# Performance work log

Measured on AMD Instinct MI355X. Metric: run time of the kernel, lower is better.

The kernel has to match this reference:

```python
import jax, jax.numpy as jnp
import numpy as np

B, S, D = 2, 2048, 2048
H, HD = 16, 128
WINDOW = 512
ROPE_BASE = 10000.0


def setup_inputs() -> dict:
    key = jax.random.key(0)
    k1, k2, k3 = jax.random.split(key, 3)
    x = jax.random.normal(k1, (B, S, D), dtype=jnp.float32)
    w_qkv = jax.random.normal(k2, (3 * D, D), dtype=jnp.float32) * (D ** -0.5)
    w_out = jax.random.normal(k3, (D, D), dtype=jnp.float32) * (D ** -0.5)
    return {"x": x, "w_qkv": w_qkv, "w_out": w_out}


def _rope_cos_sin(seq_len, head_dim, base, dtype):
    inv_freq = 1.0 / (base ** (jnp.arange(0, head_dim, 2, dtype=jnp.float32) / head_dim))
    pos = jnp.arange(seq_len, dtype=jnp.float32)
    freqs = pos[:, None] * inv_freq[None, :]            # (S, HD/2)
    emb = jnp.concatenate([freqs, freqs], axis=-1)       # (S, HD)
    return jnp.cos(emb).astype(dtype), jnp.sin(emb).astype(dtype)


def _rotate_half(x):
    x1, x2 = jnp.split(x, 2, axis=-1)
    return jnp.concatenate([-x2, x1], axis=-1)


def reference(x, w_qkv, w_out):
    Bx, Sx, Dx = x.shape
    # fused QKV projection (torch Linear: x @ W^T)
    qkv = jnp.einsum('bsd,ed->bse', x, w_qkv)
    q, k, v = jnp.split(qkv, 3, axis=-1)
    q = q.reshape(Bx, Sx, H, HD).transpose(0, 2, 1, 3)   # (B,H,S,HD)
    k = k.reshape(Bx, Sx, H, HD).transpose(0, 2, 1, 3)
    v = v.reshape(Bx, Sx, H, HD).transpose(0, 2, 1, 3)
    # RoPE with implicit position_ids = arange(S)
    cos, sin = _rope_cos_sin(Sx, HD, ROPE_BASE, x.dtype)  # (S, HD)
    q = q * cos[None, None] + _rotate_half(q) * sin[None, None]
    k = k * cos[None, None] + _rotate_half(k) * sin[None, None]
    # sliding-window attention: attend iff 0 <= i - j < WINDOW
    scale = 1.0 / jnp.sqrt(jnp.array(HD, dtype=x.dtype))
    scores = jnp.einsum('bhqd,bhkd->bhqk', q, k) * scale
    i = jnp.arange(Sx)[:, None]
    j = jnp.arange(Sx)[None, :]
    diff = i - j
    valid = (diff >= 0) & (diff < WINDOW)                # (S, S)
    scores = jnp.where(valid[None, None], scores, jnp.finfo(scores.dtype).min)
    attn = jax.nn.softmax(scores, axis=-1)
    out = jnp.einsum('bhqk,bhkd->bhqd', attn, v)
    out = out.transpose(0, 2, 1, 3).reshape(Bx, Sx, Dx)
    return jnp.einsum('bsd,ed->bse', out, w_out)
```

## Files before the change

### kernel.cpp

```cpp
#include <hip/hip_runtime.h>

#define S_LEN 2048
#define DIM 2048
#define NH 16
#define HD 128
#define WIN 512
#define QKVD (3 * DIM)

typedef unsigned short u16;
typedef unsigned int u32;
typedef __bf16 bf16x8 __attribute__((ext_vector_type(8)));
typedef float f32x4 __attribute__((ext_vector_type(4)));

__device__ __forceinline__ u16 f2bf(float f) {
  unsigned u = __builtin_bit_cast(unsigned, f);
  u += 0x7FFFu + ((u >> 16) & 1u);
  return (u16)(u >> 16);
}
__device__ __forceinline__ float bf2f(u16 b) {
  return __builtin_bit_cast(float, (unsigned)b << 16);
}
__device__ __forceinline__ void async16(const void* g, void* l) {
  __builtin_amdgcn_global_load_lds((__attribute__((address_space(1))) void*)g,
                                   (__attribute__((address_space(3))) void*)l,
                                   16, 0, 0);
}
#define WAITV(N) asm volatile("s_waitcnt vmcnt(" #N ")" ::: "memory")

__global__ __launch_bounds__(256) void cvt3_kernel(
    const float* __restrict__ a, u16* __restrict__ oa, int na,
    const float* __restrict__ b, u16* __restrict__ ob, int nb,
    const float* __restrict__ c, u16* __restrict__ oc, int nc) {
  int i = (blockIdx.x * 256 + threadIdx.x) * 4;
  const float* src;
  u16* dst;
  if (i < na) { src = a + i; dst = oa + i; }
  else if (i < na + nb) { src = b + (i - na); dst = ob + (i - na); }
  else if (i < na + nb + nc) { src = c + (i - na - nb); dst = oc + (i - na - nb); }
  else return;
  float4 v = *(const float4*)src;
  ushort4 o;
  o.x = f2bf(v.x); o.y = f2bf(v.y); o.z = f2bf(v.z); o.w = f2bf(v.w);
  *(ushort4*)dst = o;
}

__global__ __launch_bounds__(256) void rope_tab_kernel(float* __restrict__ cosT,
                                                       float* __restrict__ sinT) {
  int idx = blockIdx.x * 256 + threadIdx.x;
  int s = idx >> 6, j = idx & 63;
  double freq = exp((double)j * -0.14391156831212787);
  double a = (double)s * freq;
  cosT[idx] = (float)cos(a);
  sinT[idx] = (float)sin(a);
}

template <int BN, typename TO>
__global__ __launch_bounds__(512, 2) void gemm8(const u16* __restrict__ A,
                                                const u16* __restrict__ B,
                                                TO* __restrict__ C,
                                                int M, int N, int K) {
  constexpr int ABY = 128 * 128;
  constexpr int BBY = BN * 128;
  constexpr int BLO = BN / 128;
  __shared__ __align__(16) char Al[2 * ABY];
  __shared__ __align__(16) char Bl[2 * BBY];

  const int tiles_n = N / BN;
  const int nwg = gridDim.x;
  const int wg = ((int)blockIdx.x & 7) * (nwg >> 3) + ((int)blockIdx.x >> 3);
  const int m0 = (wg / tiles_n) << 7;
  const int n0 = (wg % tiles_n) * BN;
  const int t = threadIdx.x;
  const int l = t & 63, w = t >> 6;
  const int wr = w >> 2, wc = w & 3;
  const int l16 = l & 15, lg = l >> 4;
  const u16* Asrc = A + (size_t)m0 * K;
  const u16* Bsrc = B + (size_t)n0 * K;

  auto stA = [&](int kcol, int half, int b) {
    int rih = t >> 3, ch = t & 7;
    int row = half * 64 + rih;
    async16(Asrc + (size_t)row * K + kcol + ((ch ^ (row & 7)) << 3),
            Al + b * ABY + row * 128 + ch * 16);
  };
  auto stB = [&](int kcol, int half, int b) {
#pragma unroll
    for (int j = 0; j < BLO; ++j) {
      int c = t + j * 512;
      int rih = c >> 3, ch = c & 7;
      int row = half * (BN / 2) + rih;
      async16(Bsrc + (size_t)row * K + kcol + ((ch ^ (row & 7)) << 3),
              Bl + b * BBY + row * 128 + ch * 16);
    }
  };

  f32x4 acc[4][2 * BLO] = {};
  bf16x8 af[2][2];
  bf16x8 bfr[2][BLO][2];

  auto rdA = [&](int b, int mh) {
#pragma unroll
    for (int m = 0; m < 2; ++m)
#pragma unroll
      for (int ks = 0; ks < 2; ++ks) {
        int row = wr * 64 + mh * 32 + m * 16 + l16;
        int ch = ks * 4 + lg;
        af[m][ks] = *(const bf16x8*)(Al + b * ABY + row * 128 + ((ch ^ (row & 7)) << 4));
      }
  };
  auto rdB = [&](int b, int nh) {
#pragma unroll
    for (int n = 0; n < BLO; ++n)
#pragma unroll
      for (int ks = 0; ks < 2; ++ks) {
        int row = wc * (BN / 4) + nh * (BN / 8) + n * 16 + l16;
        int ch = ks * 4 + lg;
        bfr[nh][n][ks] = *(const bf16x8*)(Bl + b * BBY + row * 128 + ((ch ^ (row & 7)) << 4));
      }
  };
  auto mm = [&](int mh, int nh) {
#pragma unroll
    for (int m = 0; m < 2; ++m)
#pragma unroll
      for (int n = 0; n < BLO; ++n)
#pragma unroll
        for (int ks = 0; ks < 2; ++ks)
          acc[mh * 2 + m][nh * BLO + n] = __builtin_amdgcn_mfma_f32_16x16x32_bf16(
              af[m][ks], bfr[nh][n][ks], acc[mh * 2 + m][nh * BLO + n], 0, 0, 0);
  };

  const int NT = K >> 6;
  stA(0, 0, 0); stB(0, 0, 0); stB(0, 1, 0); stA(0, 1, 0); stA(64, 0, 1);
  if constexpr (BN == 384) WAITV(5); else WAITV(4);
  __builtin_amdgcn_s_barrier();

  for (int kt = 0; kt < NT; ++kt) {
    const int b = kt & 1, nb = b ^ 1;
    const int k1 = ((kt + 1 < NT) ? kt + 1 : kt) << 6;
    const int k2 = ((kt + 2 < NT) ? kt + 2 : kt) << 6;
    rdA(b, 0); rdB(b, 0);
    stB(k1, 0, nb);
    __builtin_amdgcn_s_barrier();
    __builtin_amdgcn_s_setprio(1); mm(0, 0); __builtin_amdgcn_s_setprio(0);
    if constexpr (BN == 384) WAITV(5); else WAITV(4);
    __builtin_amdgcn_s_barrier();
    rdB(b, 1);
    stB(k1, 1, nb);
    __builtin_amdgcn_s_barrier();
    __builtin_amdgcn_s_setprio(1); mm(0, 1); __builtin_amdgcn_s_setprio(0);
    if constexpr (BN == 384) WAITV(7); else WAITV(5);
    __builtin_amdgcn_s_barrier();
    rdA(b, 1);
    stA(k1, 1, nb);
    __builtin_amdgcn_s_barrier();
    __builtin_amdgcn_s_setprio(1); mm(1, 0); __builtin_amdgcn_s_setprio(0);
    __builtin_amdgcn_s_barrier();
    stA(k2, 0, b);
    __builtin_amdgcn_s_barrier();
    __builtin_amdgcn_s_setprio(1); mm(1, 1); __builtin_amdgcn_s_setprio(0);
    if constexpr (BN == 384) WAITV(5); else WAITV(4);
    __builtin_amdgcn_s_barrier();
  }

  const int rb = m0 + wr * 64 + lg * 4;
  const int cb = n0 + wc * (BN / 4) + l16;
#pragma unroll
  for (int mi = 0; mi < 4; ++mi)
#pragma unroll
    for (int ni = 0; ni < 2 * BLO; ++ni)
#pragma unroll
      for (int r = 0; r < 4; ++r) {
        float v = acc[mi][ni][r];
        size_t idx = (size_t)(rb + mi * 16 + r) * N + cb + ni * 16;
        if constexpr (sizeof(TO) == 2) C[idx] = f2bf(v);
        else C[idx] = v;
      }
}

__global__ __launch_bounds__(256) void rope_kernel(u16* __restrict__ qkv,
                                                   const float* __restrict__ cosT,
                                                   const float* __restrict__ sinT) {
  const int row = blockIdx.x;
  const int s = row & (S_LEN - 1);
  const int t = threadIdx.x;
  const int part = t >> 7;
  const int h = (t >> 3) & 15;
  const int c = t & 7;
  u16* p = qkv + (size_t)row * QKVD + part * DIM + h * HD + c * 8;
  const float* cp = cosT + (s << 6) + c * 8;
  const float* sp = sinT + (s << 6) + c * 8;
  const float4 c0 = *(const float4*)cp, c1 = *(const float4*)(cp + 4);
  const float4 s0 = *(const float4*)sp, s1 = *(const float4*)(sp + 4);
  float cs[8] = {c0.x, c0.y, c0.z, c0.w, c1.x, c1.y, c1.z, c1.w};
  float sn[8] = {s0.x, s0.y, s0.z, s0.w, s1.x, s1.y, s1.z, s1.w};
  uint4 lo = *(const uint4*)p;
  uint4 hi = *(const uint4*)(p + 64);
  unsigned lw[4] = {lo.x, lo.y, lo.z, lo.w};
  unsigned hw[4] = {hi.x, hi.y, hi.z, hi.w};
  unsigned ol[4], oh[4];
#pragma unroll
  for (int j = 0; j < 4; ++j) {
    float x1a = bf2f((u16)(lw[j] & 0xffffu)), x1b = bf2f((u16)(lw[j] >> 16));
    float x2a = bf2f((u16)(hw[j] & 0xffffu)), x2b = bf2f((u16)(hw[j] >> 16));
    float ca = cs[j * 2], cb = cs[j * 2 + 1];
    float sa = sn[j * 2], sb = sn[j * 2 + 1];
    ol[j] = (u32)f2bf(x1a * ca - x2a * sa) | ((u32)f2bf(x1b * cb - x2b * sb) << 16);
    oh[j] = (u32)f2bf(x2a * ca + x1a * sa) | ((u32)f2bf(x2b * cb + x1b * sb) << 16);
  }
  *(uint4*)p = (uint4){ol[0], ol[1], ol[2], ol[3]};
  *(uint4*)(p + 64) = (uint4){oh[0], oh[1], oh[2], oh[3]};
}

__global__ __launch_bounds__(512, 2) void attn_kernel(const u16* __restrict__ qkv,
                                                      u16* __restrict__ attnO) {
  const int bid = blockIdx.x;
  const int qt = bid & 15;
  const int bh = bid >> 4;
  const int q0 = qt << 7;
  const int b = bh >> 4, h = bh & 15;
  const u16* Qp = qkv + (size_t)b * S_LEN * QKVD + h * HD;
  const u16* Kp = Qp + DIM;
  const u16* Vp = Qp + 2 * DIM;
  __shared__ __align__(16) char Ks[2][64 * 256];
  __shared__ __align__(16) u16 Vt[128][72];
  __shared__ __align__(16) u32 Ps[8][16 * 36];
  const int t = threadIdx.x;
  const int w = t >> 6, l = t & 63;
  const int l16 = l & 15, lg = l >> 4;
  const int q0w = q0 + w * 16;
  const bf16x8 ones = __builtin_bit_cast(bf16x8,
      (uint4){0x3F803F80u, 0x3F803F80u, 0x3F803F80u, 0x3F803F80u});
  bf16x8 qf[4];
  {
    const u16* qrow = Qp + (size_t)(q0w + l16) * QKVD;
#pragma unroll
    for (int ks = 0; ks < 4; ++ks) qf[ks] = *(const bf16x8*)(qrow + ks * 32 + lg * 8);
  }
  f32x4 oacc[8] = {};
  f32x4 ldacc = {};
  const int lo = max(0, (q0 - (WIN - 1)) >> 6);
  const int hi = (q0 + 127) >> 6;
  const int lo_w = max(0, (q0w - (WIN - 1)) >> 6);
  const int hi_w = (q0w + 15) >> 6;
  const float SC2 = 0.12751744654f;
  const int qi = q0w + l16;
  const int dc = t & 15, pr_ = t >> 4;

  auto loadV = [&](int kv0, uint4& va, uint4& vb) {
    va = *(const uint4*)(Vp + (size_t)(kv0 + pr_ * 2) * QKVD + dc * 8);
    vb = *(const uint4*)(Vp + (size_t)(kv0 + pr_ * 2 + 1) * QKVD + dc * 8);
  };
  auto issueK = [&](int kv0, int buf) {
#pragma unroll
    for (int i = 0; i < 2; ++i) {
      int c = t + (i << 9);
      int row = c >> 4, ch = c & 15;
      int sch = ch ^ (row & 7);
      async16(Kp + (size_t)(kv0 + row) * QKVD + sch * 8, Ks[buf] + c * 16);
    }
  };

  uint4 va, vb, va2, vb2;
  loadV(lo << 6, va, vb);
  __builtin_amdgcn_sched_barrier(0);
  issueK(lo << 6, 0);
  __builtin_amdgcn_sched_barrier(0);

  for (int kt = lo; kt <= hi; ++kt) {
    const int buf = (kt - lo) & 1;
    const int kv0 = kt << 6;
    const int ktn = (kt < hi) ? kt + 1 : hi;
    WAITV(2);
    __builtin_amdgcn_sched_barrier(0);
    __builtin_amdgcn_s_barrier();
    {
      const int kv = pr_ * 2, d0 = dc * 8;
      unsigned av[4] = {va.x, va.y, va.z, va.w};
      unsigned bv[4] = {vb.x, vb.y, vb.z, vb.w};
#pragma unroll
      for (int j = 0; j < 4; ++j) {
        *(unsigned*)&Vt[d0 + j * 2][kv] = (av[j] & 0xffffu) | (bv[j] << 16);
        *(unsigned*)&Vt[d0 + j * 2 + 1][kv] = (av[j] >> 16) | (bv[j] & 0xffff0000u);
      }
    }
    WAITV(0);
    asm volatile("s_waitcnt lgkmcnt(0)" ::: "memory");
    __builtin_amdgcn_sched_barrier(0);
    __builtin_amdgcn_s_barrier();
    loadV(ktn << 6, va2, vb2);
    __builtin_amdgcn_sched_barrier(0);
    issueK(ktn << 6, buf ^ 1);
    __builtin_amdgcn_sched_barrier(0);
    if (kt >= lo_w && kt <= hi_w) {
      u32* pbase = &Ps[w][0];
#pragma unroll
      for (int c4 = 0; c4 < 4; ++c4) {
        f32x4 sa = {};
#pragma unroll
        for (int ks = 0; ks < 4; ++ks) {
          const int krow = c4 * 16 + l16;
          const int ch = (ks * 4 + lg) ^ (krow & 7);
          bf16x8 kf = *(const bf16x8*)(Ks[buf] + krow * 256 + ch * 16);
          sa = __builtin_amdgcn_mfma_f32_16x16x32_bf16(kf, qf[ks], sa, 0, 0, 0);
        }
        const int kj_base = kv0 + c4 * 16 + lg * 4;
        float p[4];
#pragma unroll
        for (int r = 0; r < 4; ++r) {
          unsigned diff = (unsigned)(qi - (kj_base + r));
          float v = sa[r] * SC2;
          v = (diff < WIN) ? v : -1e30f;
          p[r] = __builtin_amdgcn_exp2f(v);
        }
        const u32 w0 = (u32)f2bf(p[0]) | ((u32)f2bf(p[1]) << 16);
        const u32 w1 = (u32)f2bf(p[2]) | ((u32)f2bf(p[3]) << 16);
        const int pw = l16 * 36 + c4 * 8 + lg * 2;
        pbase[pw] = w0;
        pbase[pw + 1] = w1;
      }
      asm volatile("s_waitcnt lgkmcnt(0)" ::: "memory");
      __builtin_amdgcn_sched_barrier(0);
#pragma unroll
      for (int ks = 0; ks < 2; ++ks) {
        uint4 pr2 = *(const uint4*)&Ps[w][l16 * 36 + ks * 16 + lg * 4];
        bf16x8 pf = __builtin_bit_cast(bf16x8, pr2);
#pragma unroll
        for (int dt = 0; dt < 8; ++dt) {
          bf16x8 vf = *(const bf16x8*)(&Vt[dt * 16 + l16][ks * 32 + lg * 8]);
          oacc[dt] = __builtin_amdgcn_mfma_f32_16x16x32_bf16(pf, vf, oacc[dt], 0, 0, 0);
        }
        ldacc = __builtin_amdgcn_mfma_f32_16x16x32_bf16(pf, ones, ldacc, 0, 0, 0);
      }
    }
    va = va2; vb = vb2;
  }
  const int qr = q0w + lg * 4;
  u16* orow = attnO + ((size_t)(b * S_LEN + qr) * DIM) + h * HD;
#pragma unroll
  for (int r = 0; r < 4; ++r) {
    float inv = 1.f / ldacc[r];
#pragma unroll
    for (int dt = 0; dt < 8; ++dt)
      orow[(size_t)r * DIM + dt * 16 + l16] = f2bf(oacc[dt][r] * inv);
  }
}

extern "C" void kernel_launch(void* const* d_in, const int* in_sizes, int n_in,
                              void* d_out, int out_size, void* d_ws, size_t ws_size,
                              hipStream_t stream) {
  const float* x = (const float*)d_in[0];
  const float* w_qkv = (const float*)d_in[1];
  const float* w_out = (const float*)d_in[2];
  float* out = (float*)d_out;

  char* ws = (char*)d_ws;
  size_t off = 0;
  auto alloc = [&](size_t bytes) {
    void* p = ws + off;
    off = (off + bytes + 255) & ~(size_t)255;
    return p;
  };
  const size_t rows = 2ull * S_LEN;
  u16* wqkvb = (u16*)alloc(3ull * DIM * DIM * 2);
  u16* woutb = (u16*)alloc((size_t)DIM * DIM * 2);
  u16* xb    = (u16*)alloc(rows * DIM * 2);
  u16* qkvb  = (u16*)alloc(rows * 3 * DIM * 2);
  float* cosT = (float*)alloc((size_t)S_LEN * 64 * 4);
  float* sinT = (float*)alloc((size_t)S_LEN * 64 * 4);

  const int na = 3 * DIM * DIM, nb = DIM * DIM, nc = (int)(rows * DIM);
  cvt3_kernel<<<(na + nb + nc) / 1024, 256, 0, stream>>>(w_qkv, wqkvb, na,
                                                         w_out, woutb, nb,
                                                         x, xb, nc);
  rope_tab_kernel<<<(S_LEN * 64) / 256, 256, 0, stream>>>(cosT, sinT);
  gemm8<384, u16><<<(int)(rows / 128) * (QKVD / 384), 512, 0, stream>>>(
      xb, wqkvb, qkvb, (int)rows, QKVD, DIM);
  rope_kernel<<<(int)rows, 256, 0, stream>>>(qkvb, cosT, sinT);
  u16* attnb = wqkvb;
  attn_kernel<<<2 * NH * (S_LEN / 128), 512, 0, stream>>>(qkvb, attnb);
  gemm8<256, float><<<(int)(rows / 128) * (DIM / 256), 512, 0, stream>>>(
      attnb, woutb, out, (int)rows, DIM, DIM);
}
```

Measured before the change: 230.9 us.

## Fuse Q RoPE into attention, merge rope table into convert kernel

```diff
diff --git a/kernel.cpp b/kernel.cpp
--- a/kernel.cpp
+++ b/kernel.cpp
@@ -27,10 +27,20 @@
 }
 #define WAITV(N) asm volatile("s_waitcnt vmcnt(" #N ")" ::: "memory")
 
-__global__ __launch_bounds__(256) void cvt3_kernel(
+__global__ __launch_bounds__(256) void cvt3tab_kernel(
     const float* __restrict__ a, u16* __restrict__ oa, int na,
     const float* __restrict__ b, u16* __restrict__ ob, int nb,
-    const float* __restrict__ c, u16* __restrict__ oc, int nc) {
+    const float* __restrict__ c, u16* __restrict__ oc, int nc,
+    float* __restrict__ cosT, float* __restrict__ sinT, int nCvt) {
+  if ((int)blockIdx.x >= nCvt) {
+    int idx = ((int)blockIdx.x - nCvt) * 256 + threadIdx.x;
+    int s = idx >> 6, j = idx & 63;
+    double freq = exp((double)j * -0.14391156831212787);
+    double ang = (double)s * freq;
+    cosT[idx] = (float)cos(ang);
+    sinT[idx] = (float)sin(ang);
+    return;
+  }
   int i = (blockIdx.x * 256 + threadIdx.x) * 4;
   const float* src;
   u16* dst;
@@ -44,16 +54,6 @@
   *(ushort4*)dst = o;
 }
 
-__global__ __launch_bounds__(256) void rope_tab_kernel(float* __restrict__ cosT,
-                                                       float* __restrict__ sinT) {
-  int idx = blockIdx.x * 256 + threadIdx.x;
-  int s = idx >> 6, j = idx & 63;
-  double freq = exp((double)j * -0.14391156831212787);
-  double a = (double)s * freq;
-  cosT[idx] = (float)cos(a);
-  sinT[idx] = (float)sin(a);
-}
-
 template <int BN, typename TO>
 __global__ __launch_bounds__(512, 2) void gemm8(const u16* __restrict__ A,
                                                 const u16* __restrict__ B,
@@ -136,8 +136,8 @@
 
   for (int kt = 0; kt < NT; ++kt) {
     const int b = kt & 1, nb = b ^ 1;
-    const int k1 = ((kt + 1 < NT) ? kt + 1 : kt) << 6;
-    const int k2 = ((kt + 2 < NT) ? kt + 2 : kt) << 6;
+    const int k1 = (kt + 1) << 6;
+    const int k2 = (kt + 2) << 6;
     rdA(b, 0); rdB(b, 0);
     stB(k1, 0, nb);
     __builtin_amdgcn_s_barrier();
@@ -177,16 +177,15 @@
       }
 }
 
-__global__ __launch_bounds__(256) void rope_kernel(u16* __restrict__ qkv,
-                                                   const float* __restrict__ cosT,
-                                                   const float* __restrict__ sinT) {
-  const int row = blockIdx.x;
+__global__ __launch_bounds__(256) void ropek_kernel(u16* __restrict__ qkv,
+                                                    const float* __restrict__ cosT,
+                                                    const float* __restrict__ sinT) {
+  const int row = blockIdx.x * 2 + (threadIdx.x >> 7);
   const int s = row & (S_LEN - 1);
-  const int t = threadIdx.x;
-  const int part = t >> 7;
-  const int h = (t >> 3) & 15;
-  const int c = t & 7;
-  u16* p = qkv + (size_t)row * QKVD + part * DIM + h * HD + c * 8;
+  const int slot = threadIdx.x & 127;
+  const int h = slot >> 3;
+  const int c = slot & 7;
+  u16* p = qkv + (size_t)row * QKVD + DIM + h * HD + c * 8;
   const float* cp = cosT + (s << 6) + c * 8;
   const float* sp = sinT + (s << 6) + c * 8;
   const float4 c0 = *(const float4*)cp, c1 = *(const float4*)(cp + 4);
@@ -212,7 +211,9 @@
 }
 
 __global__ __launch_bounds__(512, 2) void attn_kernel(const u16* __restrict__ qkv,
-                                                      u16* __restrict__ attnO) {
+                                                      u16* __restrict__ attnO,
+                                                      const float* __restrict__ cosT,
+                                                      const float* __restrict__ sinT) {
   const int bid = blockIdx.x;
   const int qt = bid & 15;
   const int bh = bid >> 4;
@@ -235,6 +236,34 @@
     const u16* qrow = Qp + (size_t)(q0w + l16) * QKVD;
 #pragma unroll
     for (int ks = 0; ks < 4; ++ks) qf[ks] = *(const bf16x8*)(qrow + ks * 32 + lg * 8);
+    const int srow = q0w + l16;
+    const float* cbase = cosT + (srow << 6) + lg * 8;
+    const float* sbase = sinT + (srow << 6) + lg * 8;
+#pragma unroll
+    for (int ks = 0; ks < 2; ++ks) {
+      const float4 ca = *(const float4*)(cbase + ks * 32);
+      const float4 cb2 = *(const float4*)(cbase + ks * 32 + 4);
+      const float4 sa = *(const float4*)(sbase + ks * 32);
+      const float4 sb2 = *(const float4*)(sbase + ks * 32 + 4);
+      const float cs[8] = {ca.x, ca.y, ca.z, ca.w, cb2.x, cb2.y, cb2.z, cb2.w};
+      const float sn[8] = {sa.x, sa.y, sa.z, sa.w, sb2.x, sb2.y, sb2.z, sb2.w};
+      const uint4 lv = __builtin_bit_cast(uint4, qf[ks]);
+      const uint4 hv = __builtin_bit_cast(uint4, qf[ks + 2]);
+      const unsigned li[4] = {lv.x, lv.y, lv.z, lv.w};
+      const unsigned hi2[4] = {hv.x, hv.y, hv.z, hv.w};
+      unsigned lw[4], hw[4];
+#pragma unroll
+      for (int p2 = 0; p2 < 4; ++p2) {
+        float f1a = bf2f((u16)(li[p2] & 0xffffu)), f1b = bf2f((u16)(li[p2] >> 16));
+        float f2a = bf2f((u16)(hi2[p2] & 0xffffu)), f2b = bf2f((u16)(hi2[p2] >> 16));
+        lw[p2] = (u32)f2bf(f1a * cs[p2 * 2] - f2a * sn[p2 * 2]) |
+                 ((u32)f2bf(f1b * cs[p2 * 2 + 1] - f2b * sn[p2 * 2 + 1]) << 16);
+        hw[p2] = (u32)f2bf(f2a * cs[p2 * 2] + f1a * sn[p2 * 2]) |
+                 ((u32)f2bf(f2b * cs[p2 * 2 + 1] + f1b * sn[p2 * 2 + 1]) << 16);
+      }
+      qf[ks] = __builtin_bit_cast(bf16x8, (uint4){lw[0], lw[1], lw[2], lw[3]});
+      qf[ks + 2] = __builtin_bit_cast(bf16x8, (uint4){hw[0], hw[1], hw[2], hw[3]});
+    }
   }
   f32x4 oacc[8] = {};
   f32x4 ldacc = {};
@@ -369,15 +398,14 @@
   float* sinT = (float*)alloc((size_t)S_LEN * 64 * 4);
 
   const int na = 3 * DIM * DIM, nb = DIM * DIM, nc = (int)(rows * DIM);
-  cvt3_kernel<<<(na + nb + nc) / 1024, 256, 0, stream>>>(w_qkv, wqkvb, na,
-                                                         w_out, woutb, nb,
-                                                         x, xb, nc);
-  rope_tab_kernel<<<(S_LEN * 64) / 256, 256, 0, stream>>>(cosT, sinT);
+  const int nCvt = (na + nb + nc) / 1024;
+  cvt3tab_kernel<<<nCvt + (S_LEN * 64) / 256, 256, 0, stream>>>(
+      w_qkv, wqkvb, na, w_out, woutb, nb, x, xb, nc, cosT, sinT, nCvt);
   gemm8<384, u16><<<(int)(rows / 128) * (QKVD / 384), 512, 0, stream>>>(
       xb, wqkvb, qkvb, (int)rows, QKVD, DIM);
-  rope_kernel<<<(int)rows, 256, 0, stream>>>(qkvb, cosT, sinT);
+  ropek_kernel<<<(int)(rows / 2), 256, 0, stream>>>(qkvb, cosT, sinT);
   u16* attnb = wqkvb;
-  attn_kernel<<<2 * NH * (S_LEN / 128), 512, 0, stream>>>(qkvb, attnb);
+  attn_kernel<<<2 * NH * (S_LEN / 128), 512, 0, stream>>>(qkvb, attnb, cosT, sinT);
   gemm8<256, float><<<(int)(rows / 128) * (DIM / 256), 512, 0, stream>>>(
       attnb, woutb, out, (int)rows, DIM, DIM);
 }
```

After: 229.0 us. Within noise of the previous version (-0.8%).
